# Kernel tuning notes

Hardware: AMD Instinct MI355X
Metric: run time of the kernel (lower is better)

Reference implementation:

```python
import jax, jax.numpy as jnp
import numpy as np
from jax import lax

# module config (matches init_kwargs)
IN_CHANNELS = 1
NUM_OR = 8               # 360 / angle_res(45)
THRESHOLD = 0.9
WINDOW = (5, 5)
STRIDE = (1, 1)
WINDOW_SCALE = float(WINDOW[0] * WINDOW[1])
NORMALIZE_COUNT = True   # normalize_count=True -> avg counts (avg_pool2d semantics)


def setup_inputs() -> dict:
    key = jax.random.key(0)
    k1, k2 = jax.random.split(key)
    x = jax.random.normal(k1, (16, IN_CHANNELS, 1024, 1024), dtype=jnp.float32)
    # edge-orientation masks (Sobel rotations in the original; values are fixed
    # buffers, so random stand-ins preserve the exact compute pattern)
    masks = jax.random.normal(k2, (IN_CHANNELS * NUM_OR, 1, 3, 3), dtype=jnp.float32)
    return {"x": x, "masks": masks}


def reference(x, masks):
    # grouped edge-filter conv: [B,C,H,W] x [C*O,1,3,3] -> [B,C*O,H-2,W-2]
    y = lax.conv_general_dilated(
        x, masks, window_strides=(1, 1), padding='VALID',
        rhs_dilation=(1, 1), feature_group_count=IN_CHANNELS,
        dimension_numbers=('NCHW', 'OIHW', 'NCHW'))
    value = jnp.max(y, axis=1)    # [B,H',W']
    index = jnp.argmax(y, axis=1)  # dominant orientation per pixel
    # below-threshold responses assigned to the extra 'no edge' bin
    index = jnp.where(value < THRESHOLD, NUM_OR, index)
    # one-hot over NUM_OR+1 bins -> [B, NUM_OR+1, H', W']
    bins = (index[:, None, :, :] ==
            jnp.arange(NUM_OR + 1)[None, :, None, None]).astype(jnp.float32)
    # windowed histogram counts (avg_pool2d with no padding => plain window mean)
    counts = lax.reduce_window(bins, 0.0, lax.add,
                               (1, 1) + WINDOW, (1, 1) + STRIDE, 'VALID')
    feat = counts / WINDOW_SCALE if NORMALIZE_COUNT else counts
    return feat  # [B, NUM_OR+1, H'-4, W'-4]
```

## Files before the change

kernel.cpp:

```cpp
#include <hip/hip_runtime.h>


#define NOR 8
#define HH  1024
#define WW  1024
#define H2  1018
#define W2  1018
#define RPW 16
#define CW  60
#define NCH 17
#define PL  (H2 * W2)

__global__ __launch_bounds__(256, 4)
void ehd_wave(const float* __restrict__ x,
              const float* __restrict__ masks,
              float* __restrict__ out)
{
    const int lane  = threadIdx.x & 63;
    const int wid   = threadIdx.x >> 6;
    const int chunk = blockIdx.x * 4 + wid;
    if (chunk >= NCH) return;

    const int c0 = chunk * CW;
    const int r0 = blockIdx.y * RPW;
    const int b  = blockIdx.z;

    const float* __restrict__ xb = x + (long)b * (HH * WW);
    float* __restrict__ outb     = out + (long)b * 9 * PL;

    float m[NOR][9];
#pragma unroll
    for (int o = 0; o < NOR; ++o)
#pragma unroll
        for (int k = 0; k < 9; ++k)
            m[o][k] = masks[o * 9 + k];

    const int j  = c0 + lane;
    const int ja = j     < 1023 ? j     : 1023;
    const int jb = j + 1 < 1023 ? j + 1 : 1023;
    const int jc = j + 2 < 1023 ? j + 2 : 1023;

    float t00, t01, t02, t10, t11, t12;
    {
        const float* r = xb + r0 * WW;
        t00 = r[ja]; t01 = r[jb]; t02 = r[jc];
        r += WW;
        t10 = r[ja]; t11 = r[jb]; t12 = r[jc];
    }

    unsigned long long rs[5];

    for (int g = 0; g < 4; ++g) {
#pragma unroll
        for (int p = 0; p < 5; ++p) {
            const int it = g * 5 + p;

            int hr = r0 + it + 2; if (hr > HH - 1) hr = HH - 1;
            const float* rp = xb + hr * WW;
            const float n0 = rp[ja], n1 = rp[jb], n2 = rp[jc];

            const float xv[9] = { t00, t01, t02, t10, t11, t12, n0, n1, n2 };
            float best = 0.0f; int bi = 0;
#pragma unroll
            for (int o = 0; o < NOR; ++o) {
                float acc = xv[0] * m[o][0];
#pragma unroll
                for (int k = 1; k < 9; ++k)
                    acc = fmaf(xv[k], m[o][k], acc);
                if (o == 0)          { best = acc; bi = 0; }
                else if (acc > best) { best = acc; bi = o; }
            }
            if (best < 0.9f) bi = NOR;

            const int b1 = __shfl(bi, lane + 1);
            const int b2 = __shfl(bi, lane + 2);
            const int b3 = __shfl(bi, lane + 3);
            const int b4 = __shfl(bi, lane + 4);
            rs[p] = (1ull << (7 * bi)) + (1ull << (7 * b1)) + (1ull << (7 * b2))
                  + (1ull << (7 * b3)) + (1ull << (7 * b4));

            if (it >= 4) {
                const int ro = r0 + it - 4;
                if (ro < H2 && lane < CW && j < W2) {
                    const unsigned long long s = rs[0] + rs[1] + rs[2] + rs[3] + rs[4];
                    const unsigned off0 = (unsigned)ro * W2 + (unsigned)j;
#pragma unroll
                    for (int k = 0; k < 9; ++k) {
                        const float cv =
                            (float)((unsigned)(s >> (7 * k)) & 0x7Fu) * (1.0f / 25.0f);
                        outb[off0 + (unsigned)(k * PL)] = cv;
                    }
                }
            }

            t00 = t10; t01 = t11; t02 = t12;
            t10 = n0;  t11 = n1;  t12 = n2;
        }
    }
}

extern "C" void kernel_launch(void* const* d_in, const int* in_sizes, int n_in,
                              void* d_out, int out_size, void* d_ws, size_t ws_size,
                              hipStream_t stream)
{
    const float* x     = (const float*)d_in[0];
    const float* masks = (const float*)d_in[1];
    float* out         = (float*)d_out;

    dim3 grid((NCH + 3) / 4,
              (H2 + RPW - 1) / RPW,
              16);
    ehd_wave<<<grid, 256, 0, stream>>>(x, masks, out);
}
```

Measured before the change: 743.3 us.

## Process four columns per thread with LDS one-hot exchange and vector stores

Each block now covers a full 1024-column row band, with each thread handling four adjacent columns. Input rows are read with float4/float2 loads. The per-pixel one-hot codes go through a double-buffered shared-memory row, replacing wave shuffles, and a sliding-window prefix gives the 5-wide horizontal sums. Outputs are written as float4 stores to cut the number of store instructions and the redundant overlap loads of the old 60-of-64-lane chunking. The cost is a __syncthreads per row and float4 stores to addresses that are only 8-byte aligned.

```diff
diff --git a/kernel.cpp b/kernel.cpp
--- a/kernel.cpp
+++ b/kernel.cpp
@@ -6,27 +6,23 @@
 #define WW  1024
 #define H2  1018
 #define W2  1018
-#define RPW 16
-#define CW  60
-#define NCH 17
+#define RPB 16
 #define PL  (H2 * W2)
 
 __global__ __launch_bounds__(256, 4)
-void ehd_wave(const float* __restrict__ x,
-              const float* __restrict__ masks,
-              float* __restrict__ out)
+void ehd_r5(const float* __restrict__ x,
+            const float* __restrict__ masks,
+            float* __restrict__ out)
 {
-    const int lane  = threadIdx.x & 63;
-    const int wid   = threadIdx.x >> 6;
-    const int chunk = blockIdx.x * 4 + wid;
-    if (chunk >= NCH) return;
+    __shared__ __align__(16) unsigned long long ohrow[2][1032];
 
-    const int c0 = chunk * CW;
-    const int r0 = blockIdx.y * RPW;
-    const int b  = blockIdx.z;
+    const int t  = threadIdx.x;
+    const int j0 = t * 4;
+    const int r0 = blockIdx.x * RPB;
+    const int b  = blockIdx.y;
 
     const float* __restrict__ xb = x + (long)b * (HH * WW);
-    float* __restrict__ outb     = out + (long)b * 9 * PL;
+    float* __restrict__ outb     = out + (long)b * 9 * (long)PL;
 
     float m[NOR][9];
 #pragma unroll
@@ -35,66 +31,93 @@
         for (int k = 0; k < 9; ++k)
             m[o][k] = masks[o * 9 + k];
 
-    const int j  = c0 + lane;
-    const int ja = j     < 1023 ? j     : 1023;
-    const int jb = j + 1 < 1023 ? j + 1 : 1023;
-    const int jc = j + 2 < 1023 ? j + 2 : 1023;
+    const int jt = (j0 + 4 <= WW - 2) ? (j0 + 4) : (WW - 2);
 
-    float t00, t01, t02, t10, t11, t12;
-    {
-        const float* r = xb + r0 * WW;
-        t00 = r[ja]; t01 = r[jb]; t02 = r[jc];
-        r += WW;
-        t10 = r[ja]; t11 = r[jb]; t12 = r[jc];
-    }
+    float w0[6], w1[6], nc[6], nn[6];
+    auto loadrow = [&](int r, float* d) {
+        const float* p = xb + r * WW;
+        const float4 a = *(const float4*)(p + j0);
+        const float2 c = *(const float2*)(p + jt);
+        d[0] = a.x; d[1] = a.y; d[2] = a.z; d[3] = a.w; d[4] = c.x; d[5] = c.y;
+    };
+    loadrow(r0,     w0);
+    loadrow(r0 + 1, w1);
+    loadrow(r0 + 2, nc);
 
-    unsigned long long rs[5];
+    unsigned long long rs[5][4];
 
     for (int g = 0; g < 4; ++g) {
 #pragma unroll
-        for (int p = 0; p < 5; ++p) {
-            const int it = g * 5 + p;
+        for (int p5 = 0; p5 < 5; ++p5) {
+            const int it = g * 5 + p5;
 
-            int hr = r0 + it + 2; if (hr > HH - 1) hr = HH - 1;
-            const float* rp = xb + hr * WW;
-            const float n0 = rp[ja], n1 = rp[jb], n2 = rp[jc];
+            unsigned long long pk[4];
+#pragma unroll
+            for (int p = 0; p < 4; ++p) {
+                const float xv[9] = { w0[p], w0[p+1], w0[p+2],
+                                      w1[p], w1[p+1], w1[p+2],
+                                      nc[p], nc[p+1], nc[p+2] };
+                float best = 0.0f; int bi = 0;
+#pragma unroll
+                for (int o = 0; o < NOR; ++o) {
+                    float acc = xv[0] * m[o][0];
+#pragma unroll
+                    for (int k = 1; k < 9; ++k)
+                        acc = fmaf(xv[k], m[o][k], acc);
+                    if (o == 0)          { best = acc; bi = 0; }
+                    else if (acc > best) { best = acc; bi = o; }
+                }
+                if (best < 0.9f) bi = NOR;
+                pk[p] = 1ull << (7 * bi);
+            }
+            const int sl = it & 1;
+            { ulonglong2 v; v.x = pk[0]; v.y = pk[1]; *(ulonglong2*)&ohrow[sl][j0]     = v; }
+            { ulonglong2 v; v.x = pk[2]; v.y = pk[3]; *(ulonglong2*)&ohrow[sl][j0 + 2] = v; }
+            __syncthreads();
 
-            const float xv[9] = { t00, t01, t02, t10, t11, t12, n0, n1, n2 };
-            float best = 0.0f; int bi = 0;
-#pragma unroll
-            for (int o = 0; o < NOR; ++o) {
-                float acc = xv[0] * m[o][0];
-#pragma unroll
-                for (int k = 1; k < 9; ++k)
-                    acc = fmaf(xv[k], m[o][k], acc);
-                if (o == 0)          { best = acc; bi = 0; }
-                else if (acc > best) { best = acc; bi = o; }
-            }
-            if (best < 0.9f) bi = NOR;
+            int nr = r0 + it + 3; if (nr > HH - 1) nr = HH - 1;
+            loadrow(nr, nn);
 
-            const int b1 = __shfl(bi, lane + 1);
-            const int b2 = __shfl(bi, lane + 2);
-            const int b3 = __shfl(bi, lane + 3);
-            const int b4 = __shfl(bi, lane + 4);
-            rs[p] = (1ull << (7 * bi)) + (1ull << (7 * b1)) + (1ull << (7 * b2))
-                  + (1ull << (7 * b3)) + (1ull << (7 * b4));
+            const ulonglong2 q2 = *(const ulonglong2*)&ohrow[sl][j0 + 4];
+            const ulonglong2 q3 = *(const ulonglong2*)&ohrow[sl][j0 + 6];
+            const unsigned long long h0 = pk[0] + pk[1] + pk[2] + pk[3] + q2.x;
+            const unsigned long long h1 = h0 + q2.y - pk[0];
+            const unsigned long long h2 = h1 + q3.x - pk[1];
+            const unsigned long long h3 = h2 + q3.y - pk[2];
+            rs[p5][0] = h0; rs[p5][1] = h1; rs[p5][2] = h2; rs[p5][3] = h3;
 
             if (it >= 4) {
                 const int ro = r0 + it - 4;
-                if (ro < H2 && lane < CW && j < W2) {
-                    const unsigned long long s = rs[0] + rs[1] + rs[2] + rs[3] + rs[4];
-                    const unsigned off0 = (unsigned)ro * W2 + (unsigned)j;
+                if (ro < H2) {
+                    const unsigned long long s0 = rs[0][0]+rs[1][0]+rs[2][0]+rs[3][0]+rs[4][0];
+                    const unsigned long long s1 = rs[0][1]+rs[1][1]+rs[2][1]+rs[3][1]+rs[4][1];
+                    const unsigned long long s2 = rs[0][2]+rs[1][2]+rs[2][2]+rs[3][2]+rs[4][2];
+                    const unsigned long long s3 = rs[0][3]+rs[1][3]+rs[2][3]+rs[3][3]+rs[4][3];
+                    float* orow = outb + (unsigned)ro * W2 + j0;
+                    if (t < 254) {
 #pragma unroll
-                    for (int k = 0; k < 9; ++k) {
-                        const float cv =
-                            (float)((unsigned)(s >> (7 * k)) & 0x7Fu) * (1.0f / 25.0f);
-                        outb[off0 + (unsigned)(k * PL)] = cv;
+                        for (int k = 0; k < 9; ++k) {
+                            float4 f;
+                            f.x = (float)((unsigned)(s0 >> (7*k)) & 0x7Fu) * (1.0f/25.0f);
+                            f.y = (float)((unsigned)(s1 >> (7*k)) & 0x7Fu) * (1.0f/25.0f);
+                            f.z = (float)((unsigned)(s2 >> (7*k)) & 0x7Fu) * (1.0f/25.0f);
+                            f.w = (float)((unsigned)(s3 >> (7*k)) & 0x7Fu) * (1.0f/25.0f);
+                            *(float4*)(orow + (long)k * PL) = f;
+                        }
+                    } else if (t == 254) {
+#pragma unroll
+                        for (int k = 0; k < 9; ++k) {
+                            float2 f;
+                            f.x = (float)((unsigned)(s0 >> (7*k)) & 0x7Fu) * (1.0f/25.0f);
+                            f.y = (float)((unsigned)(s1 >> (7*k)) & 0x7Fu) * (1.0f/25.0f);
+                            *(float2*)(orow + (long)k * PL) = f;
+                        }
                     }
                 }
             }
 
-            t00 = t10; t01 = t11; t02 = t12;
-            t10 = n0;  t11 = n1;  t12 = n2;
+#pragma unroll
+            for (int d = 0; d < 6; ++d) { w0[d] = w1[d]; w1[d] = nc[d]; nc[d] = nn[d]; }
         }
     }
 }
@@ -107,8 +130,7 @@
     const float* masks = (const float*)d_in[1];
     float* out         = (float*)d_out;
 
-    dim3 grid((NCH + 3) / 4,
-              (H2 + RPW - 1) / RPW,
+    dim3 grid((H2 + RPB - 1) / RPB,
               16);
-    ehd_wave<<<grid, 256, 0, stream>>>(x, masks, out);
+    ehd_r5<<<grid, 256, 0, stream>>>(x, masks, out);
 }
```

After: 701.1 us. 5.7% less time.
